# Kernel tuning notes

Measured on AMD Instinct MI355X. Metric: run time of the kernel, lower is better.

## Reference

```python
import jax, jax.numpy as jnp
import numpy as np
from jax import lax

DN = ('NCH', 'OIH', 'NCH')

def _conv(x, w, b, pad):
    # x: [B, C, L]; replication (edge) pad then VALID conv, per nn.ReplicationPad1d + Conv1d
    if pad != (0, 0):
        x = jnp.pad(x, ((0, 0), (0, 0), pad), mode='edge')
    y = lax.conv_general_dilated(x, w, (1,), 'VALID', dimension_numbers=DN)
    return y + b[None, :, None]

def setup_inputs() -> dict:
    key = jax.random.key(0)
    ks = jax.random.split(key, 11)
    B, L, C, H = 32, 512, 300, 512
    s = 1.0 / np.sqrt(C)
    inp = {
        'x': jax.random.normal(ks[0], (B, L, C), jnp.float32),
        'w1': jax.random.normal(ks[1], (C, C, 1), jnp.float32) * s,
        'b1': jax.random.normal(ks[2], (C,), jnp.float32) * s,
        'w2': jax.random.normal(ks[3], (C, C, 2), jnp.float32) * s,
        'b2': jax.random.normal(ks[4], (C,), jnp.float32) * s,
        'w3': jax.random.normal(ks[5], (C, C, 3), jnp.float32) * s,
        'b3': jax.random.normal(ks[6], (C,), jnp.float32) * s,
        'w7': jax.random.normal(ks[7], (C, C, 7), jnp.float32) * s,
        'b7': jax.random.normal(ks[8], (C,), jnp.float32) * s,
        'slp_w': jax.random.normal(ks[9], (H, 5 * C), jnp.float32) * (1.0 / np.sqrt(5 * C)),
        'slp_b': jax.random.normal(ks[10], (H,), jnp.float32) * (1.0 / np.sqrt(5 * C)),
    }
    return inp

def reference(x, w1, b1, w2, b2, w3, b3, w7, b7, slp_w, slp_b):
    xc = jnp.transpose(x, (0, 2, 1))  # [B, C, L]
    x1 = jnp.tanh(_conv(xc, w1, b1, (0, 0)))
    x2 = jnp.tanh(_conv(xc, w2, b2, (0, 1)))
    x3 = jnp.tanh(_conv(xc, w3, b3, (1, 1)))
    x5 = x3  # faithful to the original bug: x5 = self.conv3(x)
    x7 = jnp.tanh(_conv(xc, w7, b7, (3, 3)))
    # concat channels -> [B, L, 1500], then linear + tanh -> [B, L, 512]
    h = jnp.concatenate([x1, x2, x3, x5, x7], axis=1)  # [B, 5C, L]
    h = jnp.transpose(h, (0, 2, 1))  # [B, L, 5C]
    out = jnp.tanh(jnp.einsum('blc,hc->blh', h, slp_w) + slp_b)
    return out
```

## Files before the change

kernel.cpp:

```cpp
#include <hip/hip_runtime.h>
#include <hip/hip_bf16.h>

typedef __attribute__((ext_vector_type(8))) short short8;
typedef __attribute__((ext_vector_type(16))) float floatx16;

#define Bn 32
#define Ln 512
#define Cn 300
#define Hn 512
#define Nn (Bn*Ln)
#define XBP 518
#define XBC 320
#define HK 1216
#define LDSTC 72

#define XROWS 134
#define XSZ (XROWS*LDSTC)
#define HSROWS 128
#define HSSZ (HSROWS*LDSTC)

#define XB_ELEMS (Bn*XBP*XBC)
#define WB_ELEMS 1597440
#define WC_ELEMS (Hn*HK)
#define XB_OFF 0
#define WB_OFF (XB_OFF + XB_ELEMS)
#define WC_OFF (WB_OFF + WB_ELEMS)
#define HB_OFF (WC_OFF + WC_ELEMS)

__device__ __forceinline__ float fast_tanh(float x) {
    float ax = __builtin_fabsf(x);
    float t  = __expf(-2.f * ax);
    float r  = __builtin_fmaf(-2.f * t, __frcp_rn(1.f + t), 1.f);
    return __builtin_copysignf(r, x);
}

__device__ __forceinline__ short f2bf(float v) {
    __hip_bfloat16 h = __float2bfloat16(v);
    return *reinterpret_cast<short*>(&h);
}

__global__ void prep_all(const float* __restrict__ x,
                         const float* __restrict__ w1, const float* __restrict__ w2,
                         const float* __restrict__ w3, const float* __restrict__ w7,
                         const float* __restrict__ slp_w,
                         __hip_bfloat16* __restrict__ wsb) {
    int g = blockIdx.x * 256 + threadIdx.x;
    int idx = g * 8;
    short8 o;
    if (idx < XB_ELEMS) {
        int c8 = idx % XBC;
        int t  = idx / XBC;
        int p = t % XBP;
        int b = t / XBP;
        int l = p - 3;
        l = l < 0 ? 0 : (l > Ln - 1 ? Ln - 1 : l);
        const float* row = x + (b * Ln + l) * Cn;
        if (c8 + 8 <= Cn) {
            float4 a = *(const float4*)(row + c8);
            float4 bq = *(const float4*)(row + c8 + 4);
            o[0] = f2bf(a.x); o[1] = f2bf(a.y); o[2] = f2bf(a.z); o[3] = f2bf(a.w);
            o[4] = f2bf(bq.x); o[5] = f2bf(bq.y); o[6] = f2bf(bq.z); o[7] = f2bf(bq.w);
        } else {
#pragma unroll
            for (int e = 0; e < 8; ++e) {
                int c = c8 + e;
                o[e] = f2bf(c < Cn ? row[c] : 0.f);
            }
        }
        *(short8*)&wsb[idx] = o;
    } else if (idx < WB_OFF + WB_ELEMS) {
        int r = idx - WB_OFF, taps; const float* w;
        if (r < 122880)       { taps = 1; w = w1; }
        else if (r < 368640)  { taps = 2; w = w2; r -= 122880; }
        else if (r < 737280)  { taps = 3; w = w3; r -= 368640; }
        else                  { taps = 7; w = w7; r -= 737280; }
        int lane = (r >> 3) & 63;
        int f    = (r >> 9) & 15;
        int rt   = r >> 13;
        int t    = rt % taps;
        int mc   = rt / taps;
        int ch   = mc % 5;
        int mt   = mc / 5;
        int ks = f >> 2, mq = f & 3;
        int m = mt * 128 + mq * 32 + (lane & 31);
        int cb = ch * 64 + ks * 16 + (lane >> 5) * 8;
#pragma unroll
        for (int e = 0; e < 8; ++e) {
            int c = cb + e;
            o[e] = f2bf((m < Cn && c < Cn) ? w[(m * Cn + c) * taps + t] : 0.f);
        }
        *(short8*)&wsb[idx] = o;
    } else if (idx < WC_OFF + WC_ELEMS) {
        int r = idx - WC_OFF;
        int lane = (r >> 3) & 63;
        int f    = (r >> 9) & 15;
        int mc   = r >> 13;
        int ch   = mc % 19;
        int mt4  = mc / 19;
        int ks = f >> 2, mq = f & 3;
        int h = mt4 * 128 + mq * 32 + (lane & 31);
        int kb = ch * 64 + ks * 16 + (lane >> 5) * 8;
        const float* row = slp_w + h * 1500;
#pragma unroll
        for (int e = 0; e < 8; ++e) {
            int k = kb + e;
            float v;
            if (k < 600)       v = row[k];
            else if (k < 900)  v = row[k] + row[k + 300];
            else if (k < 1200) v = row[k + 300];
            else               v = 0.f;
            o[e] = f2bf(v);
        }
        *(short8*)&wsb[idx] = o;
    }
}

#define MFMA __builtin_amdgcn_mfma_f32_32x32x16_bf16

template<int TAPS, int LEAD>
__device__ __forceinline__ void conv_body(
        const short* __restrict__ xbs, const short* __restrict__ wsp,
        const float* __restrict__ bias, int cid, int mt, int nt,
        __hip_bfloat16* __restrict__ hbuf, short* xs) {
    const int tid  = threadIdx.x;
    const int lane = tid & 63;
    const int wave = tid >> 6;
    const int wn = wave & 1, wm = wave >> 1;
    const int lr = lane & 31;
    const int lk = (lane >> 5) << 3;
    const int TRIG = (TAPS >= 3) ? TAPS - 2 : 0;

    floatx16 acc[2][2];
#pragma unroll
    for (int i = 0; i < 2; i++)
#pragma unroll
        for (int j = 0; j < 2; j++)
#pragma unroll
            for (int r = 0; r < 16; r++) acc[i][j][r] = 0.f;

    short8 bA[8], bB[8], st[5];

#pragma unroll
    for (int i = 0; i < 5; ++i) {
        int j = tid + 256 * i;
        if (i < 4 || j < 1072)
            st[i] = *(const short8*)&xbs[(j >> 3) * XBC + ((j & 7) << 3)];
    }
#pragma unroll
    for (int ks = 0; ks < 4; ++ks)
#pragma unroll
        for (int mf = 0; mf < 2; ++mf)
            bA[ks * 2 + mf] = *(const short8*)&wsp[(ks * 4 + wm * 2 + mf) * 512 + lane * 8];
#pragma unroll
    for (int i = 0; i < 5; ++i) {
        int j = tid + 256 * i;
        if (i < 4 || j < 1072)
            *(short8*)&xs[(j >> 3) * LDSTC + ((j & 7) << 3)] = st[i];
    }
    __syncthreads();

    for (int c5 = 0; c5 < 5; ++c5) {
        const short* cur = xs + (c5 & 1) * XSZ;
        short* nxt = xs + ((c5 + 1) & 1) * XSZ;
        const int c0n = (c5 + 1) * 64;
#pragma unroll
        for (int t = 0; t < TAPS; ++t) {
            if (!(c5 == 4 && t == TAPS - 1)) {
                const short* wtn = (t + 1 < TAPS) ? wsp + (c5 * TAPS + t + 1) * 8192
                                                  : wsp + ((c5 + 1) * TAPS) * 8192;
#pragma unroll
                for (int ks = 0; ks < 4; ++ks)
#pragma unroll
                    for (int mf = 0; mf < 2; ++mf)
                        bB[ks * 2 + mf] = *(const short8*)&wtn[(ks * 4 + wm * 2 + mf) * 512 + lane * 8];
            }
            if (t == TRIG && c5 < 4) {
#pragma unroll
                for (int i = 0; i < 5; ++i) {
                    int j = tid + 256 * i;
                    if (i < 4 || j < 1072)
                        st[i] = *(const short8*)&xbs[(j >> 3) * XBC + c0n + ((j & 7) << 3)];
                }
            }
            const int sh = t - LEAD + 3;
            const int ar = (wn * 64 + lr + sh) * LDSTC + lk;
#pragma unroll
            for (int ks = 0; ks < 4; ++ks) {
                short8 a0 = *(const short8*)&cur[ar + ks * 16];
                short8 a1 = *(const short8*)&cur[ar + 32 * LDSTC + ks * 16];
                acc[0][0] = MFMA(a0, bA[ks * 2 + 0], acc[0][0], 0, 0, 0);
                acc[0][1] = MFMA(a0, bA[ks * 2 + 1], acc[0][1], 0, 0, 0);
                acc[1][0] = MFMA(a1, bA[ks * 2 + 0], acc[1][0], 0, 0, 0);
                acc[1][1] = MFMA(a1, bA[ks * 2 + 1], acc[1][1], 0, 0, 0);
            }
            if (!(c5 == 4 && t == TAPS - 1)) {
#pragma unroll
                for (int f = 0; f < 8; ++f) bA[f] = bB[f];
            }
        }
        if (c5 < 4) {
#pragma unroll
            for (int i = 0; i < 5; ++i) {
                int j = tid + 256 * i;
                if (i < 4 || j < 1072)
                    *(short8*)&nxt[(j >> 3) * LDSTC + ((j & 7) << 3)] = st[i];
            }
        }
        __syncthreads();
    }

#pragma unroll
    for (int mi = 0; mi < 2; ++mi) {
        int mloc = mt * 128 + wm * 64 + mi * 32 + lr;
        int col = cid * Cn + mloc;
        if (mloc < Cn) {
            float bv = bias[mloc];
#pragma unroll
            for (int ni = 0; ni < 2; ++ni) {
                floatx16 v = acc[ni][mi];
#pragma unroll
                for (int reg = 0; reg < 16; ++reg) {
                    int nl = wn * 64 + ni * 32 + (reg & 3) + ((reg >> 2) << 3) + ((lane >> 5) << 2);
                    int n = nt * 128 + nl;
                    hbuf[n * HK + col] = __float2bfloat16(fast_tanh(v[reg] + bv));
                }
            }
        } else if (cid == 3 && col < HK) {
            __hip_bfloat16 z = __float2bfloat16(0.f);
#pragma unroll
            for (int ni = 0; ni < 2; ++ni)
#pragma unroll
                for (int reg = 0; reg < 16; ++reg) {
                    int nl = wn * 64 + ni * 32 + (reg & 3) + ((reg >> 2) << 3) + ((lane >> 5) << 2);
                    int n = nt * 128 + nl;
                    hbuf[n * HK + col] = z;
                }
        }
    }
}

__global__ __launch_bounds__(256, 2) void conv_kernel(
        const __hip_bfloat16* __restrict__ xbg, const __hip_bfloat16* __restrict__ Wbg,
        const float* __restrict__ bias1, const float* __restrict__ bias2,
        const float* __restrict__ bias3, const float* __restrict__ bias7,
        __hip_bfloat16* __restrict__ hbuf) {
    __shared__ __align__(16) short xs[2 * XSZ];

    const int nt = blockIdx.x;
    const int y  = blockIdx.y;
    const int mt = (y >= 3) ? y - 3 : y;

    const int b  = nt >> 2;
    const int l0 = (nt & 3) << 7;
    const short* xbs = (const short*)xbg + (b * XBP + l0) * XBC;
    const short* wb  = (const short*)Wbg;

    if (y < 3) {
        conv_body<7, 3>(xbs, wb + 737280 + mt * 7 * 40960, bias7, 3, mt, nt, hbuf, xs);
        conv_body<1, 0>(xbs, wb +          mt * 1 * 40960, bias1, 0, mt, nt, hbuf, xs);
    } else {
        conv_body<3, 1>(xbs, wb + 368640 + mt * 3 * 40960, bias3, 2, mt, nt, hbuf, xs);
        conv_body<2, 0>(xbs, wb + 122880 + mt * 2 * 40960, bias2, 1, mt, nt, hbuf, xs);
    }
}

__global__ __launch_bounds__(256, 2) void linear_kernel(
        const __hip_bfloat16* __restrict__ hbufg, const __hip_bfloat16* __restrict__ Wcg,
        const float* __restrict__ slp_b, float* __restrict__ out) {
    __shared__ __align__(16) short hs[2 * HSSZ];

    const int tid  = threadIdx.x;
    const int lane = tid & 63;
    const int wave = tid >> 6;
    const int wn = wave & 1, wm = wave >> 1;
    const int lr = lane & 31;
    const int lk = (lane >> 5) << 3;

    const int nt  = blockIdx.x;
    const int mt4 = blockIdx.y;

    const short* hbp = (const short*)hbufg + nt * 128 * HK;
    const short* wcp = (const short*)Wcg + mt4 * 155648;

    floatx16 acc[2][2];
#pragma unroll
    for (int i = 0; i < 2; i++)
#pragma unroll
        for (int j = 0; j < 2; j++)
#pragma unroll
            for (int r = 0; r < 16; r++) acc[i][j][r] = 0.f;

    short8 bA[8], bB[8], st[4];

#pragma unroll
    for (int i = 0; i < 4; ++i) {
        int j = tid + 256 * i;
        st[i] = *(const short8*)&hbp[(j >> 3) * HK + ((j & 7) << 3)];
    }
#pragma unroll
    for (int ks = 0; ks < 4; ++ks)
#pragma unroll
        for (int mf = 0; mf < 2; ++mf)
            bA[ks * 2 + mf] = *(const short8*)&wcp[(ks * 4 + wm * 2 + mf) * 512 + lane * 8];
#pragma unroll
    for (int i = 0; i < 4; ++i) {
        int j = tid + 256 * i;
        *(short8*)&hs[(j >> 3) * LDSTC + ((j & 7) << 3)] = st[i];
    }
    __syncthreads();

    for (int ch = 0; ch < 19; ++ch) {
        const short* cur = hs + (ch & 1) * HSSZ;
        short* nxt = hs + ((ch + 1) & 1) * HSSZ;
        if (ch < 18) {
            const short* wtn = wcp + (ch + 1) * 8192;
#pragma unroll
            for (int ks = 0; ks < 4; ++ks)
#pragma unroll
                for (int mf = 0; mf < 2; ++mf)
                    bB[ks * 2 + mf] = *(const short8*)&wtn[(ks * 4 + wm * 2 + mf) * 512 + lane * 8];
            const int c0n = (ch + 1) * 64;
#pragma unroll
            for (int i = 0; i < 4; ++i) {
                int j = tid + 256 * i;
                st[i] = *(const short8*)&hbp[(j >> 3) * HK + c0n + ((j & 7) << 3)];
            }
        }
        const int ar = (wn * 64 + lr) * LDSTC + lk;
#pragma unroll
        for (int ks = 0; ks < 4; ++ks) {
            short8 a0 = *(const short8*)&cur[ar + ks * 16];
            short8 a1 = *(const short8*)&cur[ar + 32 * LDSTC + ks * 16];
            acc[0][0] = MFMA(a0, bA[ks * 2 + 0], acc[0][0], 0, 0, 0);
            acc[0][1] = MFMA(a0, bA[ks * 2 + 1], acc[0][1], 0, 0, 0);
            acc[1][0] = MFMA(a1, bA[ks * 2 + 0], acc[1][0], 0, 0, 0);
            acc[1][1] = MFMA(a1, bA[ks * 2 + 1], acc[1][1], 0, 0, 0);
        }
        if (ch < 18) {
#pragma unroll
            for (int f = 0; f < 8; ++f) bA[f] = bB[f];
#pragma unroll
            for (int i = 0; i < 4; ++i) {
                int j = tid + 256 * i;
                *(short8*)&nxt[(j >> 3) * LDSTC + ((j & 7) << 3)] = st[i];
            }
        }
        __syncthreads();
    }

#pragma unroll
    for (int mi = 0; mi < 2; ++mi) {
        int h = mt4 * 128 + wm * 64 + mi * 32 + lr;
        float bv = slp_b[h];
#pragma unroll
        for (int ni = 0; ni < 2; ++ni) {
            floatx16 v = acc[ni][mi];
#pragma unroll
            for (int reg = 0; reg < 16; ++reg) {
                int nl = wn * 64 + ni * 32 + (reg & 3) + ((reg >> 2) << 3) + ((lane >> 5) << 2);
                int n = nt * 128 + nl;
                out[n * Hn + h] = fast_tanh(v[reg] + bv);
            }
        }
    }
}


extern "C" void kernel_launch(void* const* d_in, const int* in_sizes, int n_in,
                              void* d_out, int out_size, void* d_ws, size_t ws_size,
                              hipStream_t stream) {
    const float* x     = (const float*)d_in[0];
    const float* w1    = (const float*)d_in[1];
    const float* b1    = (const float*)d_in[2];
    const float* w2    = (const float*)d_in[3];
    const float* b2    = (const float*)d_in[4];
    const float* w3    = (const float*)d_in[5];
    const float* b3    = (const float*)d_in[6];
    const float* w7    = (const float*)d_in[7];
    const float* b7    = (const float*)d_in[8];
    const float* slp_w = (const float*)d_in[9];
    const float* slp_b = (const float*)d_in[10];

    __hip_bfloat16* wsb = (__hip_bfloat16*)d_ws;

    const int prep_groups = (XB_ELEMS + WB_ELEMS + WC_ELEMS) / 8;
    prep_all<<<(prep_groups + 255) / 256, 256, 0, stream>>>(x, w1, w2, w3, w7, slp_w, wsb);

    conv_kernel<<<dim3(128, 6), 256, 0, stream>>>(wsb + XB_OFF, wsb + WB_OFF,
                                                  b1, b2, b3, b7, wsb + HB_OFF);
    linear_kernel<<<dim3(128, 4), 256, 0, stream>>>(wsb + HB_OFF, wsb + WC_OFF,
                                                    slp_b, (float*)d_out);
}
```

Measured before the change: 204.8 us.

## Split conv kernel into one block per conv and drop LDS staging in linear kernel

The conv kernel grid grows from 6 to 12 y-blocks, so each block computes a single conv variant instead of pairing 7+1 and 3+2. This exposes more parallelism, at the cost of load imbalance between the k=7 blocks and the k=1 blocks and of reloading the x tile per block. The linear kernel no longer double-buffers the activation tile through shared memory. Each wave now reads its A fragments directly from global memory, which removes the barriers and LDS traffic but gives up reuse across waves and the explicit prefetch.

Result: slower. 218.1 us (+6.5%).

```diff
diff --git a/kernel.cpp b/kernel.cpp
--- a/kernel.cpp
+++ b/kernel.cpp
@@ -16,8 +16,6 @@
 
 #define XROWS 134
 #define XSZ (XROWS*LDSTC)
-#define HSROWS 128
-#define HSSZ (HSROWS*LDSTC)
 
 #define XB_ELEMS (Bn*XBP*XBC)
 #define WB_ELEMS 1597440
@@ -247,28 +245,24 @@
     __shared__ __align__(16) short xs[2 * XSZ];
 
     const int nt = blockIdx.x;
-    const int y  = blockIdx.y;
-    const int mt = (y >= 3) ? y - 3 : y;
+    const int my = blockIdx.y;
+    const int g  = my / 3;
+    const int mt = my % 3;
 
     const int b  = nt >> 2;
     const int l0 = (nt & 3) << 7;
     const short* xbs = (const short*)xbg + (b * XBP + l0) * XBC;
     const short* wb  = (const short*)Wbg;
 
-    if (y < 3) {
-        conv_body<7, 3>(xbs, wb + 737280 + mt * 7 * 40960, bias7, 3, mt, nt, hbuf, xs);
-        conv_body<1, 0>(xbs, wb +          mt * 1 * 40960, bias1, 0, mt, nt, hbuf, xs);
-    } else {
-        conv_body<3, 1>(xbs, wb + 368640 + mt * 3 * 40960, bias3, 2, mt, nt, hbuf, xs);
-        conv_body<2, 0>(xbs, wb + 122880 + mt * 2 * 40960, bias2, 1, mt, nt, hbuf, xs);
-    }
+    if (g == 0)      conv_body<7, 3>(xbs, wb + 737280 + mt * 7 * 40960, bias7, 3, mt, nt, hbuf, xs);
+    else if (g == 1) conv_body<3, 1>(xbs, wb + 368640 + mt * 3 * 40960, bias3, 2, mt, nt, hbuf, xs);
+    else if (g == 2) conv_body<2, 0>(xbs, wb + 122880 + mt * 2 * 40960, bias2, 1, mt, nt, hbuf, xs);
+    else             conv_body<1, 0>(xbs, wb +      0 + mt * 1 * 40960, bias1, 0, mt, nt, hbuf, xs);
 }
 
 __global__ __launch_bounds__(256, 2) void linear_kernel(
         const __hip_bfloat16* __restrict__ hbufg, const __hip_bfloat16* __restrict__ Wcg,
         const float* __restrict__ slp_b, float* __restrict__ out) {
-    __shared__ __align__(16) short hs[2 * HSSZ];
-
     const int tid  = threadIdx.x;
     const int lane = tid & 63;
     const int wave = tid >> 6;
@@ -290,62 +284,28 @@
 #pragma unroll
             for (int r = 0; r < 16; r++) acc[i][j][r] = 0.f;
 
-    short8 bA[8], bB[8], st[4];
-
-#pragma unroll
-    for (int i = 0; i < 4; ++i) {
-        int j = tid + 256 * i;
-        st[i] = *(const short8*)&hbp[(j >> 3) * HK + ((j & 7) << 3)];
-    }
-#pragma unroll
-    for (int ks = 0; ks < 4; ++ks)
-#pragma unroll
-        for (int mf = 0; mf < 2; ++mf)
-            bA[ks * 2 + mf] = *(const short8*)&wcp[(ks * 4 + wm * 2 + mf) * 512 + lane * 8];
-#pragma unroll
-    for (int i = 0; i < 4; ++i) {
-        int j = tid + 256 * i;
-        *(short8*)&hs[(j >> 3) * LDSTC + ((j & 7) << 3)] = st[i];
-    }
-    __syncthreads();
-
+    const short* a0p = hbp + (wn * 64 + lr) * HK + lk;
+    const short* a1p = a0p + 32 * HK;
+
+#pragma unroll 2
     for (int ch = 0; ch < 19; ++ch) {
-        const short* cur = hs + (ch & 1) * HSSZ;
-        short* nxt = hs + ((ch + 1) & 1) * HSSZ;
-        if (ch < 18) {
-            const short* wtn = wcp + (ch + 1) * 8192;
-#pragma unroll
-            for (int ks = 0; ks < 4; ++ks)
-#pragma unroll
-                for (int mf = 0; mf < 2; ++mf)
-                    bB[ks * 2 + mf] = *(const short8*)&wtn[(ks * 4 + wm * 2 + mf) * 512 + lane * 8];
-            const int c0n = (ch + 1) * 64;
-#pragma unroll
-            for (int i = 0; i < 4; ++i) {
-                int j = tid + 256 * i;
-                st[i] = *(const short8*)&hbp[(j >> 3) * HK + c0n + ((j & 7) << 3)];
-            }
-        }
-        const int ar = (wn * 64 + lr) * LDSTC + lk;
+        const short* wt = wcp + ch * 8192;
+        short8 b[8];
+#pragma unroll
+        for (int ks = 0; ks < 4; ++ks)
+#pragma unroll
+            for (int mf = 0; mf < 2; ++mf)
+                b[ks * 2 + mf] = *(const short8*)&wt[(ks * 4 + wm * 2 + mf) * 512 + lane * 8];
+        const int kb = ch * 64;
 #pragma unroll
         for (int ks = 0; ks < 4; ++ks) {
-            short8 a0 = *(const short8*)&cur[ar + ks * 16];
-            short8 a1 = *(const short8*)&cur[ar + 32 * LDSTC + ks * 16];
-            acc[0][0] = MFMA(a0, bA[ks * 2 + 0], acc[0][0], 0, 0, 0);
-            acc[0][1] = MFMA(a0, bA[ks * 2 + 1], acc[0][1], 0, 0, 0);
-            acc[1][0] = MFMA(a1, bA[ks * 2 + 0], acc[1][0], 0, 0, 0);
-            acc[1][1] = MFMA(a1, bA[ks * 2 + 1], acc[1][1], 0, 0, 0);
-        }
-        if (ch < 18) {
-#pragma unroll
-            for (int f = 0; f < 8; ++f) bA[f] = bB[f];
-#pragma unroll
-            for (int i = 0; i < 4; ++i) {
-                int j = tid + 256 * i;
-                *(short8*)&nxt[(j >> 3) * LDSTC + ((j & 7) << 3)] = st[i];
-            }
-        }
-        __syncthreads();
+            short8 a0 = *(const short8*)&a0p[kb + ks * 16];
+            short8 a1 = *(const short8*)&a1p[kb + ks * 16];
+            acc[0][0] = MFMA(a0, b[ks * 2 + 0], acc[0][0], 0, 0, 0);
+            acc[0][1] = MFMA(a0, b[ks * 2 + 1], acc[0][1], 0, 0, 0);
+            acc[1][0] = MFMA(a1, b[ks * 2 + 0], acc[1][0], 0, 0, 0);
+            acc[1][1] = MFMA(a1, b[ks * 2 + 1], acc[1][1], 0, 0, 0);
+        }
     }
 
 #pragma unroll
@@ -386,8 +346,8 @@
     const int prep_groups = (XB_ELEMS + WB_ELEMS + WC_ELEMS) / 8;
     prep_all<<<(prep_groups + 255) / 256, 256, 0, stream>>>(x, w1, w2, w3, w7, slp_w, wsb);
 
-    conv_kernel<<<dim3(128, 6), 256, 0, stream>>>(wsb + XB_OFF, wsb + WB_OFF,
-                                                  b1, b2, b3, b7, wsb + HB_OFF);
+    conv_kernel<<<dim3(128, 12), 256, 0, stream>>>(wsb + XB_OFF, wsb + WB_OFF,
+                                                   b1, b2, b3, b7, wsb + HB_OFF);
     linear_kernel<<<dim3(128, 4), 256, 0, stream>>>(wsb + HB_OFF, wsb + WC_OFF,
                                                     slp_b, (float*)d_out);
 }
```
